# Kernel tuning notes

Measured on AMD Instinct MI355X. Metric: run time of the kernel, lower is better.

Reference implementation:

```python
import jax, jax.numpy as jnp
import numpy as np

VOCAB = 32000
EMBED = 512


def setup_inputs() -> dict:
    key = jax.random.key(0)
    k_idx, k_w, k_b = jax.random.split(key, 3)
    input_indices = jax.random.randint(k_idx, (4, 2048), 0, VOCAB, dtype=jnp.int64)
    # Conv2d(vocab, embed, 1) weight is (embed, vocab, 1, 1); drop trailing 1x1 dims.
    fan_in = VOCAB
    bound = 1.0 / np.sqrt(fan_in)
    W = jax.random.uniform(k_w, (EMBED, VOCAB), jnp.float32, -bound, bound)
    b = jax.random.uniform(k_b, (EMBED,), jnp.float32, -bound, bound)
    return {"input_indices": input_indices, "W": W, "b": b}


def reference(input_indices, W, b):
    # Faithful to the original: one-hot encode then 1x1 conv (a dense GEMM
    # over the vocab axis), which is mathematically W[:, idx] + b.
    B, S = input_indices.shape
    one_hot = jax.nn.one_hot(input_indices, VOCAB, dtype=jnp.float32)  # [B,S,V]
    # 1x1 conv on [N, V, 1, 1] == matmul with W: [B,S,V] x [E,V] -> [B,S,E]
    embedding = jnp.einsum("bsv,ev->bse", one_hot, W) + b
    return embedding
```

## Files before the change

kernel.cpp:

```cpp
#include <hip/hip_runtime.h>
#include <hip/hip_bf16.h>


constexpr int VOCAB  = 32000;
constexpr int EMBED  = 512;
constexpr int VSHIFT = 9;
constexpr int VC     = 1 << VSHIFT;
constexpr int NCHUNK = (VOCAB + VC - 1) / VC;
constexpr int ET     = 16;
constexpr int PAD    = 516;
constexpr int CAP    = 1024;

__global__ __launch_bounds__(256) void fused_embed_kernel(
    const int* __restrict__ idx,
    const float* __restrict__ W,
    const float* __restrict__ bias,
    float* __restrict__ out,
    int ntok)
{
    __shared__ float chunk[ET * PAD];
    __shared__ int   list[CAP];
    __shared__ int   cnt;

    const int cx  = blockIdx.x;
    const int ey  = blockIdx.y;
    const int c0  = cx << VSHIFT;
    const int e0  = ey * ET;
    const int tid = threadIdx.x;

    if (tid == 0) cnt = 0;

    const int cols = min(VC, VOCAB - c0);
    const int cpr  = cols >> 8;
    const int nck  = ET * cpr;
    const int wv   = tid >> 6;
    const int lane = tid & 63;
    for (int c = wv; c < nck; c += 4) {
        int r = (cpr == 2) ? (c >> 1) : c;
        int h = (cpr == 2) ? (c & 1) : 0;
        const float* src = W + (size_t)(e0 + r) * VOCAB + c0 + (h << 8) + (lane << 2);
        float* dst = &chunk[r * PAD + (h << 8)];
        __builtin_amdgcn_global_load_lds(
            (const __attribute__((address_space(1))) void*)src,
            (__attribute__((address_space(3))) void*)dst, 16, 0, 0);
    }

    const int   j  = tid & 15;
    const float bv = bias[e0 + j];

    __syncthreads();

    const int n4 = ntok >> 2;
    const int4* idx4 = (const int4*)idx;
    for (int q = tid; q < n4; q += 256) {
        int4 v = idx4[q];
        int t = q << 2;
        if ((v.x >> VSHIFT) == cx) { int p = atomicAdd(&cnt, 1); if (p < CAP) list[p] = ((t + 0) << VSHIFT) | (v.x & (VC - 1)); }
        if ((v.y >> VSHIFT) == cx) { int p = atomicAdd(&cnt, 1); if (p < CAP) list[p] = ((t + 1) << VSHIFT) | (v.y & (VC - 1)); }
        if ((v.z >> VSHIFT) == cx) { int p = atomicAdd(&cnt, 1); if (p < CAP) list[p] = ((t + 2) << VSHIFT) | (v.z & (VC - 1)); }
        if ((v.w >> VSHIFT) == cx) { int p = atomicAdd(&cnt, 1); if (p < CAP) list[p] = ((t + 3) << VSHIFT) | (v.w & (VC - 1)); }
    }

    __syncthreads();

    const int n    = min(cnt, CAP);
    const int rowb = j * PAD;
    for (int k = tid >> 4; k < n; k += 16) {
        int e  = list[k];
        int t  = e >> VSHIFT;
        int vl = e & (VC - 1);
        float val = chunk[rowb + vl] + bv;
        __builtin_nontemporal_store(val, &out[(size_t)t * EMBED + e0 + j]);
    }
}

extern "C" void kernel_launch(void* const* d_in, const int* in_sizes, int n_in,
                              void* d_out, int out_size, void* d_ws, size_t ws_size,
                              hipStream_t stream) {
    const int*   idx  = (const int*)d_in[0];
    const float* W    = (const float*)d_in[1];
    const float* bias = (const float*)d_in[2];
    float* out = (float*)d_out;

    int ntok = in_sizes[0];

    dim3 grid(NCHUNK, EMBED / ET);
    fused_embed_kernel<<<grid, 256, 0, stream>>>(idx, W, bias, out, ntok);
}
```

Measured before the change: 105.3 us.

## Double-buffer four embed tiles per block and compact indices with wave ballots

Each block now covers 64 embedding rows instead of 16. It scans the index array once, then walks four 16-row W tiles through a two-buffer LDS pipeline: loads for the next tile are in flight while the current tile is scattered to the output. Index compaction uses per-wave ballot and popcount into per-wave segments instead of shared atomics. The aim is to cut the repeated index scans and atomic contention fourfold and to hide W load latency. In exchange the grid shrinks fourfold, LDS use roughly doubles (fewer resident blocks), and correctness depends on hand-placed waitcnt and barrier counts.

After: 107.7 us. 1.02x slower.

```diff
diff --git a/kernel.cpp b/kernel.cpp
--- a/kernel.cpp
+++ b/kernel.cpp
@@ -9,69 +9,112 @@
 constexpr int NCHUNK = (VOCAB + VC - 1) / VC;
 constexpr int ET     = 16;
 constexpr int PAD    = 516;
-constexpr int CAP    = 1024;
+constexpr int WSEG   = 512;
 
-__global__ __launch_bounds__(256) void fused_embed_kernel(
+__global__ __launch_bounds__(256) void fused_embed_pipe(
     const int* __restrict__ idx,
     const float* __restrict__ W,
     const float* __restrict__ bias,
     float* __restrict__ out,
     int ntok)
 {
-    __shared__ float chunk[ET * PAD];
-    __shared__ int   list[CAP];
-    __shared__ int   cnt;
+    __shared__ float buf[2 * ET * PAD];
+    __shared__ int   list[4 * WSEG];
+    __shared__ int   wcnts[4];
 
-    const int cx  = blockIdx.x;
-    const int ey  = blockIdx.y;
-    const int c0  = cx << VSHIFT;
-    const int e0  = ey * ET;
-    const int tid = threadIdx.x;
-
-    if (tid == 0) cnt = 0;
+    const int cx   = blockIdx.x;
+    const int c0   = cx << VSHIFT;
+    const int e0g  = blockIdx.y << 6;
+    const int tid  = threadIdx.x;
+    const int wv   = tid >> 6;
+    const int lane = tid & 63;
+    const int j    = tid & 15;
+    const int rowb = j * PAD;
 
     const int cols = min(VC, VOCAB - c0);
     const int cpr  = cols >> 8;
-    const int nck  = ET * cpr;
-    const int wv   = tid >> 6;
-    const int lane = tid & 63;
-    for (int c = wv; c < nck; c += 4) {
-        int r = (cpr == 2) ? (c >> 1) : c;
-        int h = (cpr == 2) ? (c & 1) : 0;
-        const float* src = W + (size_t)(e0 + r) * VOCAB + c0 + (h << 8) + (lane << 2);
-        float* dst = &chunk[r * PAD + (h << 8)];
-        __builtin_amdgcn_global_load_lds(
-            (const __attribute__((address_space(1))) void*)src,
-            (__attribute__((address_space(3))) void*)dst, 16, 0, 0);
-    }
+    float* bA = buf;
+    float* bB = buf + ET * PAD;
 
-    const int   j  = tid & 15;
-    const float bv = bias[e0 + j];
+    auto issue_tile = [&](float* dst, int e0t) {
+        for (int c = wv; c < 32; c += 4) {
+            int r    = c >> 1;
+            int h    = c & 1;
+            int hoff = (h & (cpr - 1)) << 8;
+            const float* src = W + (size_t)(e0t + r) * VOCAB + c0 + hoff + (lane << 2);
+            __builtin_amdgcn_global_load_lds(
+                (const __attribute__((address_space(1))) void*)src,
+                (__attribute__((address_space(3))) void*)(dst + r * PAD + (h << 8)),
+                16, 0, 0);
+        }
+    };
 
-    __syncthreads();
+    auto scatter_tile = [&](const float* b, float bv, int e0t) {
+        for (int w = 0; w < 4; ++w) {
+            int nw = wcnts[w];
+            const int* seg = list + w * WSEG;
+            for (int k = tid >> 4; k < nw; k += 16) {
+                int e   = seg[k];
+                int tok = e >> VSHIFT;
+                int vl  = e & (VC - 1);
+                float val = b[rowb + vl] + bv;
+                __builtin_nontemporal_store(val, &out[(size_t)tok * EMBED + e0t + j]);
+            }
+        }
+    };
 
-    const int n4 = ntok >> 2;
-    const int4* idx4 = (const int4*)idx;
-    for (int q = tid; q < n4; q += 256) {
-        int4 v = idx4[q];
-        int t = q << 2;
-        if ((v.x >> VSHIFT) == cx) { int p = atomicAdd(&cnt, 1); if (p < CAP) list[p] = ((t + 0) << VSHIFT) | (v.x & (VC - 1)); }
-        if ((v.y >> VSHIFT) == cx) { int p = atomicAdd(&cnt, 1); if (p < CAP) list[p] = ((t + 1) << VSHIFT) | (v.y & (VC - 1)); }
-        if ((v.z >> VSHIFT) == cx) { int p = atomicAdd(&cnt, 1); if (p < CAP) list[p] = ((t + 2) << VSHIFT) | (v.z & (VC - 1)); }
-        if ((v.w >> VSHIFT) == cx) { int p = atomicAdd(&cnt, 1); if (p < CAP) list[p] = ((t + 3) << VSHIFT) | (v.w & (VC - 1)); }
+    issue_tile(bA, e0g);
+
+    const float bv0 = bias[e0g + j];
+    const float bv1 = bias[e0g + 16 + j];
+    const float bv2 = bias[e0g + 32 + j];
+    const float bv3 = bias[e0g + 48 + j];
+
+    {
+        int wbase = 0;
+        const int n4 = ntok >> 2;
+        const int4* idx4 = (const int4*)idx;
+        for (int q = tid; q < n4; q += 256) {
+            int4 v = idx4[q];
+            int t = q << 2;
+            unsigned long long lt = (1ull << lane) - 1;
+            #pragma unroll
+            for (int s = 0; s < 4; ++s) {
+                int vi = (s == 0) ? v.x : (s == 1) ? v.y : (s == 2) ? v.z : v.w;
+                bool m = ((vi >> VSHIFT) == cx);
+                unsigned long long bm = __ballot(m);
+                if (m) {
+                    int p = wbase + __popcll(bm & lt);
+                    if (p < WSEG) list[wv * WSEG + p] = ((t + s) << VSHIFT) | (vi & (VC - 1));
+                }
+                wbase += __popcll(bm);
+            }
+        }
+        if (lane == 0) wcnts[wv] = min(wbase, WSEG);
     }
 
     __syncthreads();
 
-    const int n    = min(cnt, CAP);
-    const int rowb = j * PAD;
-    for (int k = tid >> 4; k < n; k += 16) {
-        int e  = list[k];
-        int t  = e >> VSHIFT;
-        int vl = e & (VC - 1);
-        float val = chunk[rowb + vl] + bv;
-        __builtin_nontemporal_store(val, &out[(size_t)t * EMBED + e0 + j]);
-    }
+    issue_tile(bB, e0g + 16);
+    scatter_tile(bA, bv0, e0g);
+    asm volatile("s_waitcnt lgkmcnt(0)" ::: "memory");
+    __builtin_amdgcn_s_barrier();
+
+    issue_tile(bA, e0g + 32);
+    asm volatile("s_waitcnt vmcnt(8)" ::: "memory");
+    __builtin_amdgcn_s_barrier();
+    scatter_tile(bB, bv1, e0g + 16);
+    asm volatile("s_waitcnt lgkmcnt(0)" ::: "memory");
+    __builtin_amdgcn_s_barrier();
+
+    issue_tile(bB, e0g + 48);
+    asm volatile("s_waitcnt vmcnt(8)" ::: "memory");
+    __builtin_amdgcn_s_barrier();
+    scatter_tile(bA, bv2, e0g + 32);
+
+    asm volatile("s_waitcnt vmcnt(0)" ::: "memory");
+    __builtin_amdgcn_s_barrier();
+    scatter_tile(bB, bv3, e0g + 48);
 }
 
 extern "C" void kernel_launch(void* const* d_in, const int* in_sizes, int n_in,
@@ -84,6 +127,6 @@
 
     int ntok = in_sizes[0];
 
-    dim3 grid(NCHUNK, EMBED / ET);
-    fused_embed_kernel<<<grid, 256, 0, stream>>>(idx, W, bias, out, ntok);
+    dim3 grid(NCHUNK, EMBED / 64);
+    fused_embed_pipe<<<grid, 256, 0, stream>>>(idx, W, bias, out, ntok);
 }
```
